# Kernel tuning notes

Hardware: AMD Instinct MI355X
Metric: run time of the kernel (lower is better)

## Reference

```python
import jax, jax.numpy as jnp
import numpy as np

B, N, D, H = 4, 1024, 1024, 16
DH = D // H
MLP = 4 * D
EPS = 1e-6


def setup_inputs() -> dict:
    key = jax.random.key(0)
    ks = jax.random.split(key, 16)
    s = lambda fan_in: 1.0 / np.sqrt(fan_in)
    inp = {
        "x": jax.random.normal(ks[0], (B, N, D), jnp.float32),
        "c": jax.random.normal(ks[1], (B, D), jnp.float32),
        # weights stored (in, out); torch Linear is x @ W.T + b
        "Wq": jax.random.normal(ks[2], (D, D), jnp.float32) * s(D),
        "bq": jnp.zeros((D,), jnp.float32),
        "Wkv": jax.random.normal(ks[3], (D, 2 * D), jnp.float32) * s(D),
        "bkv": jnp.zeros((2 * D,), jnp.float32),
        "Wo": jax.random.normal(ks[4], (D, D), jnp.float32) * s(D),
        "bo": jnp.zeros((D,), jnp.float32),
        "W1": jax.random.normal(ks[5], (D, MLP), jnp.float32) * s(D),
        "b1": jnp.zeros((MLP,), jnp.float32),
        "W2": jax.random.normal(ks[6], (MLP, D), jnp.float32) * s(MLP),
        "b2": jnp.zeros((D,), jnp.float32),
        "Wada": jax.random.normal(ks[7], (D, 6 * D), jnp.float32) * s(D),
        "bada": jnp.zeros((6 * D,), jnp.float32),
    }
    return inp


def _layernorm(h):
    mu = jnp.mean(h, axis=-1, keepdims=True)
    var = jnp.mean(jnp.square(h - mu), axis=-1, keepdims=True)
    return (h - mu) / jnp.sqrt(var + EPS)


def _modulate(h, shift, scale):
    return h * (1.0 + scale[:, None, :]) + shift[:, None, :]


def reference(x, c, Wq, bq, Wkv, bkv, Wo, bo, W1, b1, W2, b2, Wada, bada):
    scale = DH ** -0.5
    mod = jax.nn.silu(c) @ Wada + bada  # [B, 6D]
    sh_msa, sc_msa, g_msa, sh_mlp, sc_mlp, g_mlp = jnp.split(mod, 6, axis=-1)

    # --- attention branch ---
    h = _modulate(_layernorm(x), sh_msa, sc_msa)
    q = (h @ Wq + bq).reshape(B, N, H, DH)
    kv = h @ Wkv + bkv
    k, v = jnp.split(kv, 2, axis=-1)
    k = k.reshape(B, N, H, DH)
    v = v.reshape(B, N, H, DH)
    sim = jnp.einsum("bihd,bjhd->bhij", q, k) * scale  # [B,H,N,N]
    attn = jax.nn.softmax(sim, axis=-1)
    out = jnp.einsum("bhij,bjhd->bihd", attn, v).reshape(B, N, D)
    out = out @ Wo + bo
    x = x + g_msa[:, None, :] * out

    # --- MLP branch ---
    h2 = _modulate(_layernorm(x), sh_mlp, sc_mlp)
    m = jax.nn.gelu(h2 @ W1 + b1, approximate=True) @ W2 + b2
    x = x + g_mlp[:, None, :] * m
    return x
```

## Files before the change

### kernel.cpp

```cpp
#include <hip/hip_runtime.h>
#include <hip/hip_bf16.h>
#include <cstdint>

typedef __attribute__((ext_vector_type(4))) float f32x4;
typedef __attribute__((ext_vector_type(16))) float f32x16;
typedef __attribute__((ext_vector_type(8))) short s16x8;
typedef __attribute__((ext_vector_type(4))) unsigned u32x4;
typedef unsigned short u16;

#define B_  4
#define N_  1024
#define D_  1024
#define H_  16
#define DH_ 64
#define M_  4096
#define SIXD 6144

#define WAITV(n) asm volatile("s_waitcnt vmcnt(" #n ")" ::: "memory")

__device__ __forceinline__ u16 f2bf(float f) {
    unsigned u = __builtin_bit_cast(unsigned, f);
    unsigned r = (u + 0x7fffu + ((u >> 16) & 1u)) >> 16;
    return (u16)r;
}

__device__ __forceinline__ unsigned cvtpk(float a, float b) {
    unsigned r;
    asm("v_cvt_pk_bf16_f32 %0, %1, %2" : "=v"(r) : "v"(a), "v"(b));
    return r;
}

__device__ __forceinline__ void gload16(const void* g, void* l) {
    __builtin_amdgcn_global_load_lds((const __attribute__((address_space(1))) void*)g,
                                     (__attribute__((address_space(3))) void*)l,
                                     16, 0, 0);
}

__global__ __launch_bounds__(256) void prep_all(const float* __restrict__ Wq,
                                                const float* __restrict__ Wkv,
                                                const float* __restrict__ Wo,
                                                const float* __restrict__ W1,
                                                const float* __restrict__ W2,
                                                const float* __restrict__ c,
                                                const float* __restrict__ Wada,
                                                u16* __restrict__ wqkvT,
                                                u16* __restrict__ woT,
                                                u16* __restrict__ w1T,
                                                u16* __restrict__ w2T,
                                                float* __restrict__ modp) {
    int id = blockIdx.x;
    int tid = threadIdx.x;
    if (id < 768) {
        __shared__ float sc[128];
        int colblk = id % 24, b = (id / 24) & 3, ks = id / 96;
        int col = colblk * 256 + tid;
        int k0 = ks * 128;
        if (tid < 128) {
            float v = c[b * D_ + k0 + tid];
            sc[tid] = v / (1.f + __expf(-v));
        }
        __syncthreads();
        float a0 = 0.f, a1 = 0.f, a2 = 0.f, a3 = 0.f;
#pragma unroll 4
        for (int k = 0; k < 128; k += 4) {
            a0 = fmaf(sc[k + 0], Wada[(size_t)(k0 + k + 0) * SIXD + col], a0);
            a1 = fmaf(sc[k + 1], Wada[(size_t)(k0 + k + 1) * SIXD + col], a1);
            a2 = fmaf(sc[k + 2], Wada[(size_t)(k0 + k + 2) * SIXD + col], a2);
            a3 = fmaf(sc[k + 3], Wada[(size_t)(k0 + k + 3) * SIXD + col], a3);
        }
        modp[(size_t)(ks * 4 + b) * SIXD + col] = (a0 + a1) + (a2 + a3);
        return;
    }
    int t_ = id - 768;
    const float* in; u16* outp; int R, C, loc;
    if (t_ < 256)       { in = Wq;  outp = wqkvT;           R = 1024; C = 1024; loc = t_; }
    else if (t_ < 768)  { in = Wkv; outp = wqkvT + 1048576; R = 1024; C = 2048; loc = t_ - 256; }
    else if (t_ < 1024) { in = Wo;  outp = woT;             R = 1024; C = 1024; loc = t_ - 768; }
    else if (t_ < 2048) { in = W1;  outp = w1T;             R = 1024; C = 4096; loc = t_ - 1024; }
    else                { in = W2;  outp = w2T;             R = 4096; C = 1024; loc = t_ - 2048; }
    int tpc = C >> 6;
    int bx = loc % tpc, by = loc / tpc;
    __shared__ float t[64][65];
    int r0 = by * 64, c0 = bx * 64;
    int cx = tid & 63, ry = tid >> 6;
#pragma unroll
    for (int i = 0; i < 16; ++i) {
        int rr = ry + 4 * i;
        t[rr][cx] = in[(size_t)(r0 + rr) * C + c0 + cx];
    }
    __syncthreads();
#pragma unroll
    for (int i = 0; i < 16; ++i) {
        int cc = ry + 4 * i;
        outp[(size_t)(c0 + cc) * R + r0 + cx] = f2bf(t[cx][cc]);
    }
}

__global__ __launch_bounds__(256) void reduce_mod(const float* __restrict__ modp,
                                                  const float* __restrict__ bada,
                                                  float* __restrict__ mod) {
    int col = blockIdx.x * 256 + threadIdx.x;
    int b = blockIdx.y;
    float s = bada[col];
#pragma unroll
    for (int ks = 0; ks < 8; ++ks)
        s += modp[(size_t)(ks * 4 + b) * SIXD + col];
    mod[b * SIXD + col] = s;
}

__global__ __launch_bounds__(256) void ln_mod(const float* __restrict__ x,
                                              const float* __restrict__ mod,
                                              int shift_c, int scale_c,
                                              u16* __restrict__ h) {
    int row = blockIdx.x;
    int b = row >> 10;
    int tid = threadIdx.x, w = tid >> 6;
    float4 xv = ((const float4*)(x + (size_t)row * D_))[tid];
    float s  = xv.x + xv.y + xv.z + xv.w;
    float s2 = xv.x * xv.x + xv.y * xv.y + xv.z * xv.z + xv.w * xv.w;
#pragma unroll
    for (int m = 1; m <= 32; m <<= 1) { s += __shfl_xor(s, m); s2 += __shfl_xor(s2, m); }
    __shared__ float red[8];
    if ((tid & 63) == 0) { red[w * 2] = s; red[w * 2 + 1] = s2; }
    __syncthreads();
    float S  = red[0] + red[2] + red[4] + red[6];
    float S2 = red[1] + red[3] + red[5] + red[7];
    float mu = S * (1.f / D_);
    float var = S2 * (1.f / D_) - mu * mu;
    float rstd = rsqrtf(var + 1e-6f);
    int d0 = tid * 4;
    float4 shv = *(const float4*)(mod + b * SIXD + shift_c * D_ + d0);
    float4 scv = *(const float4*)(mod + b * SIXD + scale_c * D_ + d0);
    ushort4 o;
    o.x = f2bf((xv.x - mu) * rstd * (1.f + scv.x) + shv.x);
    o.y = f2bf((xv.y - mu) * rstd * (1.f + scv.y) + shv.y);
    o.z = f2bf((xv.z - mu) * rstd * (1.f + scv.z) + shv.z);
    o.w = f2bf((xv.w - mu) * rstd * (1.f + scv.w) + shv.w);
    *(ushort4*)(h + (size_t)row * D_ + d0) = o;
}

__global__ __launch_bounds__(256) void gemm_qkv(const u16* __restrict__ A,
                                                const u16* __restrict__ Bt,
                                                const float* __restrict__ bias,
                                                const float* __restrict__ bias2,
                                                u16* __restrict__ out,
                                                int M, int Nn, int K) {
    __shared__ char lds[2][32768];
    const int tid = threadIdx.x;
    const int w = tid >> 6, lane = tid & 63;
    const int li = lane & 15, lg = lane >> 4;
    const int nwg = gridDim.x * gridDim.y;
    const int flat = blockIdx.y * gridDim.x + blockIdx.x;
    const int wg = (flat & 7) * (nwg >> 3) + (flat >> 3);
    const int m0 = (wg / gridDim.x) * 128, n0 = (wg % gridDim.x) * 128;
    const int wr = w >> 1, wc = w & 1;

    f32x4 acc[4][4];
#pragma unroll
    for (int i = 0; i < 4; ++i)
#pragma unroll
        for (int j = 0; j < 4; ++j) acc[i][j] = (f32x4){0.f, 0.f, 0.f, 0.f};

    auto STAGE = [&](int kk, char* buf) {
#pragma unroll
        for (int j = 0; j < 8; ++j) {
            int basec = j * 256 + w * 64;
            int idx = basec + lane;
            int idl = idx & 1023;
            int row = idl >> 3, cc = idl & 7;
            const u16* src;
            if (idx < 1024)
                src = A + (size_t)(m0 + row) * K + kk + ((cc ^ (row & 7)) << 3);
            else
                src = Bt + (size_t)(n0 + row) * K + kk + ((cc ^ (row & 7)) << 3);
            gload16(src, buf + basec * 16);
        }
    };

    const int nt = K >> 6;
    STAGE(0, lds[0]);
    __syncthreads();
    int cur = 0;
    for (int t = 0; t < nt; ++t) {
        if (t + 1 < nt) { STAGE((t + 1) << 6, lds[cur ^ 1]); WAITV(8); }
        else WAITV(0);
        __builtin_amdgcn_s_barrier();
        __builtin_amdgcn_sched_barrier(0);
        const char* Ab = lds[cur];
        const char* Bb = lds[cur] + 16384;
#pragma unroll
        for (int hh = 0; hh < 2; ++hh) {
            s16x8 af[4], bfr[4];
#pragma unroll
            for (int mi = 0; mi < 4; ++mi) {
                int r = wr * 64 + mi * 16 + li;
                af[mi] = *(const s16x8*)(Ab + r * 128 + (((hh * 4 + lg) ^ (r & 7)) << 4));
            }
#pragma unroll
            for (int nj = 0; nj < 4; ++nj) {
                int r = wc * 64 + nj * 16 + li;
                bfr[nj] = *(const s16x8*)(Bb + r * 128 + (((hh * 4 + lg) ^ (r & 7)) << 4));
            }
#pragma unroll
            for (int mi = 0; mi < 4; ++mi)
#pragma unroll
                for (int nj = 0; nj < 4; ++nj)
                    acc[mi][nj] = __builtin_amdgcn_mfma_f32_16x16x32_bf16(
                        af[mi], bfr[nj], acc[mi][nj], 0, 0, 0);
        }
        __builtin_amdgcn_s_barrier();
        cur ^= 1;
    }

#pragma unroll
    for (int mi = 0; mi < 4; ++mi) {
#pragma unroll
        for (int nj = 0; nj < 4; ++nj) {
            int col = n0 + wc * 64 + nj * 16 + li;
            float bv = (col < D_) ? bias[col] : bias2[col - D_];
#pragma unroll
            for (int rg = 0; rg < 4; ++rg) {
                int grow = m0 + wr * 64 + mi * 16 + 4 * lg + rg;
                float v = acc[mi][nj][rg] + bv;
                int b = grow >> 10, n = grow & 1023;
                if (col < D_) {
                    int hd = col >> 6, dh = col & 63;
                    out[(((size_t)(b * H_ + hd)) * N_ + n) * DH_ + dh] = f2bf(v);
                } else if (col < 2 * D_) {
                    int c2 = col - D_;
                    int hd = c2 >> 6, dh = c2 & 63;
                    out[4194304u + (((size_t)(b * H_ + hd)) * N_ + n) * DH_ + dh] = f2bf(v);
                } else {
                    int c2 = col - 2 * D_;
                    int hd = c2 >> 6, dh = c2 & 63;
                    out[8388608u + (((size_t)(b * H_ + hd)) * DH_ + dh) * N_ + n] = f2bf(v);
                }
            }
        }
    }
}

template <int EPI>
__global__ __launch_bounds__(256) void gemm_bt(const u16* __restrict__ A,
                                               const u16* __restrict__ Bt,
                                               const float* __restrict__ bias,
                                               void* __restrict__ out,
                                               const float* __restrict__ xres,
                                               const float* __restrict__ mod,
                                               int M, int Nn, int K, int gate_c) {
    __shared__ char lds[2][32768];
    const int tid = threadIdx.x;
    const int w = tid >> 6, lane = tid & 63;
    const int li = lane & 15, lg = lane >> 4;
    const int nwg = gridDim.x * gridDim.y;
    const int flat = blockIdx.y * gridDim.x + blockIdx.x;
    const int wg = (flat & 7) * (nwg >> 3) + (flat >> 3);
    const int m0 = (wg / gridDim.x) * 128, n0 = (wg % gridDim.x) * 128;
    const int wr = w >> 1, wc = w & 1;

    f32x4 acc[4][4];
#pragma unroll
    for (int i = 0; i < 4; ++i)
#pragma unroll
        for (int j = 0; j < 4; ++j) acc[i][j] = (f32x4){0.f, 0.f, 0.f, 0.f};

    auto STAGE = [&](int kk, char* buf) {
#pragma unroll
        for (int j = 0; j < 8; ++j) {
            int basec = j * 256 + w * 64;
            int idx = basec + lane;
            int idl = idx & 1023;
            int row = idl >> 3, cc = idl & 7;
            const u16* src;
            if (idx < 1024)
                src = A + (size_t)(m0 + row) * K + kk + ((cc ^ (row & 7)) << 3);
            else
                src = Bt + (size_t)(n0 + row) * K + kk + ((cc ^ (row & 7)) << 3);
            gload16(src, buf + basec * 16);
        }
    };

    const int nt = K >> 6;
    STAGE(0, lds[0]);
    __syncthreads();
    int cur = 0;
    for (int t = 0; t < nt; ++t) {
        if (t + 1 < nt) { STAGE((t + 1) << 6, lds[cur ^ 1]); WAITV(8); }
        else WAITV(0);
        __builtin_amdgcn_s_barrier();
        __builtin_amdgcn_sched_barrier(0);
        const char* Ab = lds[cur];
        const char* Bb = lds[cur] + 16384;
#pragma unroll
        for (int hh = 0; hh < 2; ++hh) {
            s16x8 af[4], bfr[4];
#pragma unroll
            for (int mi = 0; mi < 4; ++mi) {
                int r = wr * 64 + mi * 16 + li;
                af[mi] = *(const s16x8*)(Ab + r * 128 + (((hh * 4 + lg) ^ (r & 7)) << 4));
            }
#pragma unroll
            for (int nj = 0; nj < 4; ++nj) {
                int r = wc * 64 + nj * 16 + li;
                bfr[nj] = *(const s16x8*)(Bb + r * 128 + (((hh * 4 + lg) ^ (r & 7)) << 4));
            }
#pragma unroll
            for (int mi = 0; mi < 4; ++mi)
#pragma unroll
                for (int nj = 0; nj < 4; ++nj)
                    acc[mi][nj] = __builtin_amdgcn_mfma_f32_16x16x32_bf16(
                        af[mi], bfr[nj], acc[mi][nj], 0, 0, 0);
        }
        __builtin_amdgcn_s_barrier();
        cur ^= 1;
    }

#pragma unroll
    for (int mi = 0; mi < 4; ++mi) {
#pragma unroll
        for (int nj = 0; nj < 4; ++nj) {
            int col = n0 + wc * 64 + nj * 16 + li;
            float bv = bias[col];
#pragma unroll
            for (int rg = 0; rg < 4; ++rg) {
                int grow = m0 + wr * 64 + mi * 16 + 4 * lg + rg;
                float v = acc[mi][nj][rg] + bv;
                int b = grow >> 10;
                size_t off = (size_t)grow * D_ + col;
                float g = mod[b * SIXD + gate_c * D_ + col];
                ((float*)out)[off] = xres[off] + g * v;
            }
        }
    }
}

__global__ __launch_bounds__(512, 2) void gemm256_gelu(const u16* __restrict__ A,
                                                       const u16* __restrict__ Bt,
                                                       const float* __restrict__ bias,
                                                       u16* __restrict__ out,
                                                       int M, int Nn, int K) {
    __shared__ char lds[2][65536];
    const int tid = threadIdx.x;
    const int w = tid >> 6, lane = tid & 63;
    const int li = lane & 15, lg = lane >> 4;
    const int wr = w >> 1, wc = w & 1;

    const int flat = blockIdx.x;
    const int wg = (flat & 7) * 32 + (flat >> 3);
    const int mg = wg >> 6, r_ = wg & 63;
    const int mt = mg * 4 + (r_ & 3), nt_ = r_ >> 2;
    const int m0 = mt * 256, n0 = nt_ * 256;

    f32x4 acc[4][8];
#pragma unroll
    for (int i = 0; i < 4; ++i)
#pragma unroll
        for (int j = 0; j < 8; ++j) acc[i][j] = (f32x4){0.f, 0.f, 0.f, 0.f};

    auto STAGE = [&](int kk, char* buf) {
#pragma unroll
        for (int j = 0; j < 4; ++j) {
            int basec = j * 512 + w * 64;
            int idx = basec + lane;
            int row = idx >> 3, cc = idx & 7;
            gload16(A + (size_t)(m0 + row) * K + kk + ((cc ^ (row & 7)) << 3),
                    buf + basec * 16);
            gload16(Bt + (size_t)(n0 + row) * K + kk + ((cc ^ (row & 7)) << 3),
                    buf + 32768 + basec * 16);
        }
    };

    const int nt = K >> 6;
    STAGE(0, lds[0]);
    __syncthreads();
    int cur = 0;
    for (int t = 0; t < nt; ++t) {
        if (t + 1 < nt) STAGE((t + 1) << 6, lds[cur ^ 1]);
        const char* Ab = lds[cur];
        const char* Bb = lds[cur] + 32768;
#pragma unroll
        for (int hh = 0; hh < 2; ++hh) {
            s16x8 af[4], bfr[8];
#pragma unroll
            for (int mi = 0; mi < 4; ++mi) {
                int r = wr * 64 + mi * 16 + li;
                af[mi] = *(const s16x8*)(Ab + r * 128 + (((hh * 4 + lg) ^ (r & 7)) << 4));
            }
#pragma unroll
            for (int nj = 0; nj < 8; ++nj) {
                int r = wc * 128 + nj * 16 + li;
                bfr[nj] = *(const s16x8*)(Bb + r * 128 + (((hh * 4 + lg) ^ (r & 7)) << 4));
            }
#pragma unroll
            for (int mi = 0; mi < 4; ++mi)
#pragma unroll
                for (int nj = 0; nj < 8; ++nj)
                    acc[mi][nj] = __builtin_amdgcn_mfma_f32_16x16x32_bf16(
                        af[mi], bfr[nj], acc[mi][nj], 0, 0, 0);
        }
        __syncthreads();
        cur ^= 1;
    }

#pragma unroll
    for (int nj = 0; nj < 8; ++nj) {
        int col = n0 + wc * 128 + nj * 16 + li;
        float bv = bias[col];
#pragma unroll
        for (int mi = 0; mi < 4; ++mi) {
#pragma unroll
            for (int rg = 0; rg < 4; ++rg) {
                int grow = m0 + wr * 64 + mi * 16 + 4 * lg + rg;
                float v = acc[mi][nj][rg] + bv;
                float u = 0.7978845608028654f * v * (1.f + 0.044715f * v * v);
                u = fminf(fmaxf(u, -15.f), 15.f);
                float e = __expf(2.f * u);
                float th = (e - 1.f) / (e + 1.f);
                out[(size_t)grow * (size_t)Nn + col] = f2bf(0.5f * v * (1.f + th));
            }
        }
    }
}

__global__ __launch_bounds__(256) void attn2(const u16* __restrict__ q,
                                             const u16* __restrict__ k,
                                             const u16* __restrict__ vt,
                                             u16* __restrict__ o) {
    __shared__ __align__(16) char qs[16384];
    __shared__ __align__(16) char kv[2][16384];
    const int tid = threadIdx.x, w = tid >> 6, lane = tid & 63;
    const int l31 = lane & 31, hi = lane >> 5;
    const int flat = blockIdx.x;
    const int wgs = (flat & 7) * 64 + (flat >> 3);
    const int bh = wgs >> 3, qt = wgs & 7;
    const size_t base = (size_t)bh * (N_ * DH_);
    const int q0 = qt * 128;

#pragma unroll
    for (int j = 0; j < 4; ++j) {
        int basec = j * 256 + w * 64;
        int idx = basec + lane;
        int row = idx >> 3, cc = idx & 7;
        gload16(q + base + (size_t)(q0 + row) * DH_ + ((cc ^ (row & 7)) << 3),
                qs + basec * 16);
    }
    auto STAGEKV = [&](int t, char* buf) {
#pragma unroll
        for (int j = 0; j < 4; ++j) {
            int basec = j * 256 + w * 64;
            int idx = basec + lane;
            if (idx < 512) {
                int row = idx >> 3, cc = idx & 7;
                gload16(k + base + (size_t)(t * 64 + row) * DH_ + ((cc ^ (row & 7)) << 3),
                        buf + basec * 16);
            } else {
                int i2 = idx - 512;
                int row = i2 >> 3, cc = i2 & 7;
                gload16(vt + base + (size_t)row * N_ + t * 64 + ((cc ^ (row & 7)) << 3),
                        buf + basec * 16);
            }
        }
    };
    STAGEKV(0, kv[0]);
    __syncthreads();

    s16x8 qf[4];
    const int qr = w * 32 + l31;
#pragma unroll
    for (int st = 0; st < 4; ++st)
        qf[st] = *(const s16x8*)(qs + qr * 128 + (((st * 2 + hi) ^ (qr & 7)) << 4));

    f32x16 oa[2];
#pragma unroll
    for (int r = 0; r < 16; ++r) { oa[0][r] = 0.f; oa[1][r] = 0.f; }
    float mrow = -3e38f, lrow = 0.f;
    const float CSC = 0.125f * 1.44269504088896f;

    int cur = 0;
    for (int t = 0; t < 16; ++t) {
        if (t + 1 < 16) STAGEKV(t + 1, kv[cur ^ 1]);
        const char* Kb = kv[cur];
        const char* Vb = kv[cur] + 8192;

        f32x16 s[2];
#pragma unroll
        for (int r = 0; r < 16; ++r) { s[0][r] = 0.f; s[1][r] = 0.f; }
#pragma unroll
        for (int st = 0; st < 4; ++st) {
#pragma unroll
            for (int ks = 0; ks < 2; ++ks) {
                int r = ks * 32 + l31;
                s16x8 ka = *(const s16x8*)(Kb + r * 128 + (((st * 2 + hi) ^ (r & 7)) << 4));
                s[ks] = __builtin_amdgcn_mfma_f32_32x32x16_bf16(ka, qf[st], s[ks], 0, 0, 0);
            }
        }

        float tmax = s[0][0];
#pragma unroll
        for (int r = 1; r < 16; ++r) tmax = fmaxf(tmax, s[0][r]);
#pragma unroll
        for (int r = 0; r < 16; ++r) tmax = fmaxf(tmax, s[1][r]);
        tmax = fmaxf(tmax, __shfl_xor(tmax, 32));
        float mn = fmaxf(mrow, tmax);
        float al = __builtin_amdgcn_exp2f((mrow - mn) * CSC);
        float nmc = -mn * CSC;
        float rs0 = 0.f, rs1 = 0.f;
#pragma unroll
        for (int r = 0; r < 16; ++r) {
            float p0 = __builtin_amdgcn_exp2f(fmaf(s[0][r], CSC, nmc));
            float p1 = __builtin_amdgcn_exp2f(fmaf(s[1][r], CSC, nmc));
            s[0][r] = p0; s[1][r] = p1;
            rs0 += p0; rs1 += p1;
        }
        float rs = rs0 + rs1;
        rs += __shfl_xor(rs, 32);
        lrow = lrow * al + rs;
        mrow = mn;
#pragma unroll
        for (int r = 0; r < 16; ++r) { oa[0][r] *= al; oa[1][r] *= al; }

        unsigned u[16];
#pragma unroll
        for (int ks = 0; ks < 2; ++ks)
#pragma unroll
            for (int j = 0; j < 4; ++j) {
                u[ks * 8 + 2 * j]     = cvtpk(s[ks][4 * j + 0], s[ks][4 * j + 1]);
                u[ks * 8 + 2 * j + 1] = cvtpk(s[ks][4 * j + 2], s[ks][4 * j + 3]);
            }

#pragma unroll
        for (int kstep = 0; kstep < 4; ++kstep) {
            unsigned b0 = u[kstep * 4 + 0], b1 = u[kstep * 4 + 1];
            unsigned b2 = u[kstep * 4 + 2], b3 = u[kstep * 4 + 3];
            asm volatile("v_permlane32_swap_b32 %0, %1" : "+v"(b0), "+v"(b2));
            asm volatile("v_permlane32_swap_b32 %0, %1" : "+v"(b1), "+v"(b3));
            u32x4 pbu = (u32x4){b0, b1, b2, b3};
            s16x8 pb = __builtin_bit_cast(s16x8, pbu);
#pragma unroll
            for (int ds = 0; ds < 2; ++ds) {
                int r = ds * 32 + l31;
                s16x8 va = *(const s16x8*)(Vb + r * 128 + (((kstep * 2 + hi) ^ (r & 7)) << 4));
                oa[ds] = __builtin_amdgcn_mfma_f32_32x32x16_bf16(va, pb, oa[ds], 0, 0, 0);
            }
        }
        __syncthreads();
        cur ^= 1;
    }

    float inv = 1.f / lrow;
#pragma unroll
    for (int ds = 0; ds < 2; ++ds)
#pragma unroll
        for (int j = 0; j < 4; ++j)
#pragma unroll
            for (int t2 = 0; t2 < 2; ++t2) {
                unsigned pk = cvtpk(oa[ds][4 * j + 2 * t2] * inv,
                                    oa[ds][4 * j + 2 * t2 + 1] * inv);
                int row = qr;
                int dch = 4 * ds + j;
                *(unsigned*)(qs + row * 128 + ((dch ^ (row & 7)) << 4) +
                             (4 * hi + 2 * t2) * 2) = pk;
            }
    __syncthreads();
    {
        int r = tid >> 1, h2 = tid & 1;
        const int b = bh >> 4, hd = bh & 15;
        size_t obase = ((size_t)(b * N_ + q0 + r)) * D_ + hd * DH_;
#pragma unroll
        for (int c = 0; c < 4; ++c) {
            int c2 = h2 * 4 + c;
            s16x8 v = *(const s16x8*)(qs + r * 128 + ((c2 ^ (r & 7)) << 4));
            *(s16x8*)(o + obase + c2 * 8) = v;
        }
    }
}

extern "C" void kernel_launch(void* const* d_in, const int* in_sizes, int n_in,
                              void* d_out, int out_size, void* d_ws, size_t ws_size,
                              hipStream_t stream) {
    const float* x    = (const float*)d_in[0];
    const float* c    = (const float*)d_in[1];
    const float* Wq   = (const float*)d_in[2];
    const float* bq   = (const float*)d_in[3];
    const float* Wkv  = (const float*)d_in[4];
    const float* bkv  = (const float*)d_in[5];
    const float* Wo   = (const float*)d_in[6];
    const float* bo   = (const float*)d_in[7];
    const float* W1   = (const float*)d_in[8];
    const float* b1   = (const float*)d_in[9];
    const float* W2   = (const float*)d_in[10];
    const float* b2   = (const float*)d_in[11];
    const float* Wada = (const float*)d_in[12];
    const float* bada = (const float*)d_in[13];

    char* ws = (char*)d_ws;
    const size_t MB = 1024 * 1024;
    u16*   wqkvT = (u16*)(ws + 0);
    u16*   woT  = (u16*)(ws + 6 * MB);
    u16*   w1T  = (u16*)(ws + 8 * MB);
    u16*   w2T  = (u16*)(ws + 16 * MB);
    float* mod  = (float*)(ws + 24 * MB);
    float* modp = (float*)(ws + 24 * MB + 131072);
    u16*   h    = (u16*)(ws + 25 * MB);
    u16*   qb   = (u16*)(ws + 33 * MB);
    u16*   ao   = (u16*)(ws + 57 * MB);
    float* x1   = (float*)(ws + 65 * MB);
    u16*   m1   = (u16*)(ws + 33 * MB);
    float* outp = (float*)d_out;

    prep_all<<<3840, 256, 0, stream>>>(Wq, Wkv, Wo, W1, W2, c, Wada,
                                       wqkvT, woT, w1T, w2T, modp);
    reduce_mod<<<dim3(24, 4), 256, 0, stream>>>(modp, bada, mod);

    ln_mod<<<M_, 256, 0, stream>>>(x, mod, 0, 1, h);

    gemm_qkv<<<dim3(24, 32), 256, 0, stream>>>(h, wqkvT, bq, bkv, qb, M_, 3 * D_, D_);

    attn2<<<512, 256, 0, stream>>>(qb, qb + 4194304, qb + 8388608, ao);

    gemm_bt<2><<<dim3(8, 32), 256, 0, stream>>>(ao, woT, bo, x1, x, mod, M_, D_, D_, 2);

    ln_mod<<<M_, 256, 0, stream>>>(x1, mod, 3, 4, h);

    gemm256_gelu<<<256, 512, 0, stream>>>(h, w1T, b1, m1, M_, 4 * D_, D_);
    gemm_bt<4><<<dim3(8, 32), 256, 0, stream>>>(m1, w2T, b2, outp, x1, mod, M_, D_, 4 * D_, 5);
}
```

Measured before the change: 220.6 us.

## Retile QKV GEMM to 256x256 blocks with 512 threads and XCD-aware mapping

Replaces the 128x128-tile QKV projection GEMM with a 256x256-tile kernel using 8 waves per block, 64 KB double-buffered LDS stages and a 4x8 MFMA accumulator per wave. Blocks are mapped so that each XCD works on a contiguous group of M and N tiles, to improve L2 reuse of the operands. The explicit vmcnt wait plus barrier is replaced by a single __syncthreads at the end of each iteration, which lets the next-stage loads overlap the current compute. The tradeoff is that the launch shrinks to 192 blocks, which is fewer than the number of CUs, and register pressure rises from the larger accumulator.

After: 220.4 us. About the same (-0.1%).

```diff
diff --git a/kernel.cpp b/kernel.cpp
--- a/kernel.cpp
+++ b/kernel.cpp
@@ -139,41 +139,40 @@
     *(ushort4*)(h + (size_t)row * D_ + d0) = o;
 }
 
-__global__ __launch_bounds__(256) void gemm_qkv(const u16* __restrict__ A,
-                                                const u16* __restrict__ Bt,
-                                                const float* __restrict__ bias,
-                                                const float* __restrict__ bias2,
-                                                u16* __restrict__ out,
-                                                int M, int Nn, int K) {
-    __shared__ char lds[2][32768];
+__global__ __launch_bounds__(512, 2) void gemm256_qkv(const u16* __restrict__ A,
+                                                      const u16* __restrict__ Bt,
+                                                      const float* __restrict__ bias,
+                                                      const float* __restrict__ bias2,
+                                                      u16* __restrict__ out,
+                                                      int M, int Nn, int K) {
+    __shared__ char lds[2][65536];
     const int tid = threadIdx.x;
     const int w = tid >> 6, lane = tid & 63;
     const int li = lane & 15, lg = lane >> 4;
-    const int nwg = gridDim.x * gridDim.y;
-    const int flat = blockIdx.y * gridDim.x + blockIdx.x;
-    const int wg = (flat & 7) * (nwg >> 3) + (flat >> 3);
-    const int m0 = (wg / gridDim.x) * 128, n0 = (wg % gridDim.x) * 128;
     const int wr = w >> 1, wc = w & 1;
 
-    f32x4 acc[4][4];
+    const int flat = blockIdx.x;
+    const int xcd = flat & 7, r_ = flat >> 3;
+    const int mt = (xcd >> 1) * 4 + (r_ & 3);
+    const int nt_ = (xcd & 1) * 6 + (r_ >> 2);
+    const int m0 = mt * 256, n0 = nt_ * 256;
+
+    f32x4 acc[4][8];
 #pragma unroll
     for (int i = 0; i < 4; ++i)
 #pragma unroll
-        for (int j = 0; j < 4; ++j) acc[i][j] = (f32x4){0.f, 0.f, 0.f, 0.f};
+        for (int j = 0; j < 8; ++j) acc[i][j] = (f32x4){0.f, 0.f, 0.f, 0.f};
 
     auto STAGE = [&](int kk, char* buf) {
 #pragma unroll
-        for (int j = 0; j < 8; ++j) {
-            int basec = j * 256 + w * 64;
+        for (int j = 0; j < 4; ++j) {
+            int basec = j * 512 + w * 64;
             int idx = basec + lane;
-            int idl = idx & 1023;
-            int row = idl >> 3, cc = idl & 7;
-            const u16* src;
-            if (idx < 1024)
-                src = A + (size_t)(m0 + row) * K + kk + ((cc ^ (row & 7)) << 3);
-            else
-                src = Bt + (size_t)(n0 + row) * K + kk + ((cc ^ (row & 7)) << 3);
-            gload16(src, buf + basec * 16);
+            int row = idx >> 3, cc = idx & 7;
+            gload16(A + (size_t)(m0 + row) * K + kk + ((cc ^ (row & 7)) << 3),
+                    buf + basec * 16);
+            gload16(Bt + (size_t)(n0 + row) * K + kk + ((cc ^ (row & 7)) << 3),
+                    buf + 32768 + basec * 16);
         }
     };
 
@@ -182,42 +181,39 @@
     __syncthreads();
     int cur = 0;
     for (int t = 0; t < nt; ++t) {
-        if (t + 1 < nt) { STAGE((t + 1) << 6, lds[cur ^ 1]); WAITV(8); }
-        else WAITV(0);
-        __builtin_amdgcn_s_barrier();
-        __builtin_amdgcn_sched_barrier(0);
+        if (t + 1 < nt) STAGE((t + 1) << 6, lds[cur ^ 1]);
         const char* Ab = lds[cur];
-        const char* Bb = lds[cur] + 16384;
+        const char* Bb = lds[cur] + 32768;
 #pragma unroll
         for (int hh = 0; hh < 2; ++hh) {
-            s16x8 af[4], bfr[4];
+            s16x8 af[4], bfr[8];
 #pragma unroll
             for (int mi = 0; mi < 4; ++mi) {
                 int r = wr * 64 + mi * 16 + li;
                 af[mi] = *(const s16x8*)(Ab + r * 128 + (((hh * 4 + lg) ^ (r & 7)) << 4));
             }
 #pragma unroll
-            for (int nj = 0; nj < 4; ++nj) {
-                int r = wc * 64 + nj * 16 + li;
+            for (int nj = 0; nj < 8; ++nj) {
+                int r = wc * 128 + nj * 16 + li;
                 bfr[nj] = *(const s16x8*)(Bb + r * 128 + (((hh * 4 + lg) ^ (r & 7)) << 4));
             }
 #pragma unroll
             for (int mi = 0; mi < 4; ++mi)
 #pragma unroll
-                for (int nj = 0; nj < 4; ++nj)
+                for (int nj = 0; nj < 8; ++nj)
                     acc[mi][nj] = __builtin_amdgcn_mfma_f32_16x16x32_bf16(
                         af[mi], bfr[nj], acc[mi][nj], 0, 0, 0);
         }
-        __builtin_amdgcn_s_barrier();
+        __syncthreads();
         cur ^= 1;
     }
 
 #pragma unroll
-    for (int mi = 0; mi < 4; ++mi) {
-#pragma unroll
-        for (int nj = 0; nj < 4; ++nj) {
-            int col = n0 + wc * 64 + nj * 16 + li;
-            float bv = (col < D_) ? bias[col] : bias2[col - D_];
+    for (int nj = 0; nj < 8; ++nj) {
+        int col = n0 + wc * 128 + nj * 16 + li;
+        float bv = (col < D_) ? bias[col] : bias2[col - D_];
+#pragma unroll
+        for (int mi = 0; mi < 4; ++mi) {
 #pragma unroll
             for (int rg = 0; rg < 4; ++rg) {
                 int grow = m0 + wr * 64 + mi * 16 + 4 * lg + rg;
@@ -614,7 +610,7 @@
 
     ln_mod<<<M_, 256, 0, stream>>>(x, mod, 0, 1, h);
 
-    gemm_qkv<<<dim3(24, 32), 256, 0, stream>>>(h, wqkvT, bq, bkv, qb, M_, 3 * D_, D_);
+    gemm256_qkv<<<192, 512, 0, stream>>>(h, wqkvT, bq, bkv, qb, M_, 3 * D_, D_);
 
     attn2<<<512, 256, 0, stream>>>(qb, qb + 4194304, qb + 8388608, ao);
 
```
